# Kernel tuning notes

Hardware: AMD Instinct MI355X
Metric: run time of the kernel (lower is better)

Reference implementation:

```python
import jax, jax.numpy as jnp
import numpy as np

D_MODEL = 1024
NUM_HEADS = 16
DEPTH = D_MODEL // NUM_HEADS
B, S = 4, 1024


def setup_inputs() -> dict:
    key = jax.random.key(0)
    ks = jax.random.split(key, 9)
    scale = 0.02
    return {
        "v": jax.random.normal(ks[0], (B, S, D_MODEL), jnp.float32),
        "k": jax.random.normal(ks[1], (B, S, D_MODEL), jnp.float32),
        "q": jax.random.normal(ks[2], (B, S, D_MODEL), jnp.float32),
        "wq_w": jax.random.normal(ks[3], (D_MODEL, D_MODEL), jnp.float32) * scale,
        "wq_b": jax.random.normal(ks[4], (D_MODEL,), jnp.float32) * scale,
        "wv_w": jax.random.normal(ks[5], (D_MODEL, D_MODEL), jnp.float32) * scale,
        "wv_b": jax.random.normal(ks[6], (D_MODEL,), jnp.float32) * scale,
        "dense_w": jax.random.normal(ks[7], (D_MODEL, D_MODEL), jnp.float32) * scale,
        "dense_b": jax.random.normal(ks[8], (D_MODEL,), jnp.float32) * scale,
    }


def _split_heads(x):
    # [B, S, D] -> [B, H, S, depth]
    b, s, _ = x.shape
    return x.reshape(b, s, NUM_HEADS, DEPTH).transpose(0, 2, 1, 3)


def reference(v, k, q, wq_w, wq_b, wv_w, wv_b, dense_w, dense_b):
    # Faithful to original torch module, including its bugs:
    #   v = wv(v); k = wv(v)  (k input and wk layer unused)
    #   output = logits @ v   (raw logits, NOT softmax weights)
    del k  # unused in original forward (overwritten)
    q_p = q @ wq_w.T + wq_b
    v_p = v @ wv_w.T + wv_b
    k_p = v_p @ wv_w.T + wv_b  # k = self.wv(v) after v already projected

    qh = _split_heads(q_p)  # [B,H,S,dh]
    kh = _split_heads(k_p)
    vh = _split_heads(v_p)

    logits = jnp.einsum("bhsd,bhtd->bhst", qh, kh) / jnp.sqrt(
        jnp.asarray(DEPTH, jnp.float32)
    )  # [B,H,S,S]
    attention_weights = jax.nn.softmax(logits, axis=-1)
    # BUG preserved: uses logits, not attention_weights
    attn_out = jnp.einsum("bhst,bhtd->bhsd", logits, vh)  # [B,H,S,dh]

    concat = attn_out.transpose(0, 2, 1, 3).reshape(B, S, D_MODEL)
    output = concat @ dense_w.T + dense_b
    # dropout is identity in eval mode
    return output, attention_weights
```

## Files before the change

kernel.cpp:

```cpp
#include <hip/hip_runtime.h>
#include <hip/hip_bf16.h>

#define DM 1024
#define BS 4
#define SS 1024
#define NH 16

typedef __attribute__((ext_vector_type(8))) short bf16x8;
typedef __attribute__((ext_vector_type(4))) float f32x4;

__device__ inline unsigned short f2bf(float x) {
    union { float f; unsigned u; } v; v.f = x;
    unsigned r = v.u + 0x7fffu + ((v.u >> 16) & 1u);
    return (unsigned short)(r >> 16);
}
__device__ inline float bf2f(unsigned short u) {
    union { unsigned u; float f; } v; v.u = ((unsigned)u) << 16;
    return v.f;
}

template<typename T> __device__ inline void store1(T* p, float v);
template<> __device__ inline void store1<float>(float* p, float v) { *p = v; }
template<> __device__ inline void store1<unsigned short>(unsigned short* p, float v) { *p = f2bf(v); }

__device__ inline void glds16(const unsigned short* g, unsigned short* l) {
    __builtin_amdgcn_global_load_lds(
        (const __attribute__((address_space(1))) unsigned int*)g,
        (__attribute__((address_space(3))) unsigned int*)l, 16, 0, 0);
}

__global__ __launch_bounds__(256) void cvt_bf16(const float* __restrict__ in,
                                                unsigned short* __restrict__ out, int n4)
{
    int i = blockIdx.x * blockDim.x + threadIdx.x;
    const int stride = gridDim.x * blockDim.x;
    for (; i < n4; i += stride) {
        float4 v = reinterpret_cast<const float4*>(in)[i];
        ushort4 o;
        o.x = f2bf(v.x); o.y = f2bf(v.y); o.z = f2bf(v.z); o.w = f2bf(v.w);
        reinterpret_cast<ushort4*>(out)[i] = o;
    }
}

template<typename TO>
__global__ __launch_bounds__(256) void gemm64_bt(
    const unsigned short* __restrict__ A, int lda,
    const unsigned short* __restrict__ B, int ldb,
    TO* __restrict__ C, int ldc,
    const float* __restrict__ bias, int K, float scale)
{
    __shared__ unsigned short lA[2][64 * 32];
    __shared__ unsigned short lB[2][64 * 32];

    const int tid = threadIdx.x;
    const int wid = tid >> 6, lane = tid & 63;
    const int wr = wid >> 1, wc = wid & 1;
    const int r0 = lane & 15;
    const int kq = (lane >> 4) * 8;
    const int srow = lane >> 2;
    const int scol = (lane & 3) * 8;

    const unsigned short* Ap = A + ((long long)blockIdx.y * 64 + wid * 16 + srow) * lda + scol;
    const unsigned short* Bp = B + ((long long)blockIdx.x * 64 + wid * 16 + srow) * ldb + scol;
    TO* Cp = C + (long long)blockIdx.y * 64 * ldc + blockIdx.x * 64;

    f32x4 acc[2][2];
    #pragma unroll
    for (int m = 0; m < 2; ++m)
        #pragma unroll
        for (int n = 0; n < 2; ++n)
            acc[m][n] = f32x4{0.f, 0.f, 0.f, 0.f};

    glds16(Ap, &lA[0][wid * 512]);
    glds16(Bp, &lB[0][wid * 512]);
    __syncthreads();

    const int NT = K / 32;
    int cur = 0;
    for (int t = 0; t < NT; ++t) {
        if (t + 1 < NT) {
            glds16(Ap + (t + 1) * 32, &lA[cur ^ 1][wid * 512]);
            glds16(Bp + (t + 1) * 32, &lB[cur ^ 1][wid * 512]);
        }
        bf16x8 af[2], bfr[2];
        #pragma unroll
        for (int m = 0; m < 2; ++m)
            af[m] = *reinterpret_cast<const bf16x8*>(&lA[cur][(wr * 32 + m * 16 + r0) * 32 + kq]);
        #pragma unroll
        for (int n = 0; n < 2; ++n)
            bfr[n] = *reinterpret_cast<const bf16x8*>(&lB[cur][(wc * 32 + n * 16 + r0) * 32 + kq]);
        #pragma unroll
        for (int m = 0; m < 2; ++m)
            #pragma unroll
            for (int n = 0; n < 2; ++n)
                acc[m][n] = __builtin_amdgcn_mfma_f32_16x16x32_bf16(af[m], bfr[n], acc[m][n], 0, 0, 0);
        __syncthreads();
        cur ^= 1;
    }

    const int cf = lane & 15, rf = (lane >> 4) * 4;
    #pragma unroll
    for (int m = 0; m < 2; ++m) {
        #pragma unroll
        for (int n = 0; n < 2; ++n) {
            int col = wc * 32 + n * 16 + cf;
            float bv = bias ? bias[blockIdx.x * 64 + col] : 0.0f;
            #pragma unroll
            for (int j = 0; j < 4; ++j) {
                int row = wr * 32 + m * 16 + rf + j;
                store1<TO>(&Cp[(long long)row * ldc + col], acc[m][n][j] * scale + bv);
            }
        }
    }
}

__global__ __launch_bounds__(256) void transpose_vh(const unsigned short* __restrict__ vp,
                                                    unsigned short* __restrict__ vT)
{
    __shared__ unsigned short tile[64][65];
    const int bh = blockIdx.y;
    const int b = bh >> 4, h = bh & 15;
    const long long t0 = (long long)blockIdx.x * 64;
    const int tid = threadIdx.x;
    #pragma unroll
    for (int kk = 0; kk < 4; ++kk) {
        int l = tid + kk * 256;
        int row = l >> 4, c4 = l & 15;
        const unsigned short* src = vp + ((long long)b * SS + t0 + row) * DM + h * 64 + c4 * 4;
        ushort4 val = *reinterpret_cast<const ushort4*>(src);
        tile[row][c4 * 4 + 0] = val.x;
        tile[row][c4 * 4 + 1] = val.y;
        tile[row][c4 * 4 + 2] = val.z;
        tile[row][c4 * 4 + 3] = val.w;
    }
    __syncthreads();
    #pragma unroll
    for (int kk = 0; kk < 4; ++kk) {
        int l = tid + kk * 256;
        int d = l >> 4, i4 = l & 15;
        ushort4 o;
        o.x = tile[i4 * 4 + 0][d];
        o.y = tile[i4 * 4 + 1][d];
        o.z = tile[i4 * 4 + 2][d];
        o.w = tile[i4 * 4 + 3][d];
        *reinterpret_cast<ushort4*>(vT + ((long long)bh * 64 + d) * SS + t0 + i4 * 4) = o;
    }
}

__global__ __launch_bounds__(256, 4) void fused_attn3(
    const unsigned short* __restrict__ qp,
    const unsigned short* __restrict__ kp,
    const unsigned short* __restrict__ vT,
    float* __restrict__ attnw,
    unsigned short* __restrict__ cc)
{
    constexpr int LSTR = 1032;
    __shared__ alignas(16) unsigned short S16[16 * LSTR];
    __shared__ float2 msW[4][16];
    __shared__ float rowM[16];
    __shared__ float rowI[16];

    const int tid = threadIdx.x;
    const int w = tid >> 6;
    const int lane = tid & 63;
    const int lg = lane >> 4;
    const int ln = lane & 15;
    const int z = blockIdx.y, b = z >> 4, h = z & 15;
    const int row0 = blockIdx.x * 16;

    const unsigned short* qbase = qp + ((long long)b * SS + row0) * DM + h * 64;
    const unsigned short* kbase = kp + (long long)b * SS * DM + h * 64;
    const unsigned short* vbase = vT + (long long)z * 64 * SS;

    bf16x8 qf[2];
    #pragma unroll
    for (int ks = 0; ks < 2; ++ks)
        qf[ks] = *reinterpret_cast<const bf16x8*>(qbase + (long long)ln * DM + ks * 32 + lg * 8);

    float m4[4], s4[4];
    #pragma unroll
    for (int j = 0; j < 4; ++j) { m4[j] = -1e30f; s4[j] = 0.f; }

    bf16x8 kf_cur[4];
    #pragma unroll
    for (int i = 0; i < 4; ++i) {
        const int ks = i >> 1, cf2 = i & 1;
        kf_cur[i] = *reinterpret_cast<const bf16x8*>(
            kbase + (long long)(w * 32 + cf2 * 16 + ln) * DM + ks * 32 + lg * 8);
    }
    for (int c = 0; c < 8; ++c) {
        bf16x8 kf_nxt[4];
        if (c < 7) {
            #pragma unroll
            for (int i = 0; i < 4; ++i) {
                const int ks = i >> 1, cf2 = i & 1;
                kf_nxt[i] = *reinterpret_cast<const bf16x8*>(
                    kbase + (long long)((c + 1) * 128 + w * 32 + cf2 * 16 + ln) * DM + ks * 32 + lg * 8);
            }
        }
        f32x4 sac[2];
        sac[0] = f32x4{0.f, 0.f, 0.f, 0.f};
        sac[1] = f32x4{0.f, 0.f, 0.f, 0.f};
        sac[0] = __builtin_amdgcn_mfma_f32_16x16x32_bf16(qf[0], kf_cur[0], sac[0], 0, 0, 0);
        sac[1] = __builtin_amdgcn_mfma_f32_16x16x32_bf16(qf[0], kf_cur[1], sac[1], 0, 0, 0);
        sac[0] = __builtin_amdgcn_mfma_f32_16x16x32_bf16(qf[1], kf_cur[2], sac[0], 0, 0, 0);
        sac[1] = __builtin_amdgcn_mfma_f32_16x16x32_bf16(qf[1], kf_cur[3], sac[1], 0, 0, 0);

        const int colbase = c * 128 + w * 32;
        #pragma unroll
        for (int cf2 = 0; cf2 < 2; ++cf2)
            #pragma unroll
            for (int j = 0; j < 4; ++j) {
                unsigned short ub = f2bf(sac[cf2][j] * 0.125f);
                S16[(lg * 4 + j) * LSTR + colbase + cf2 * 16 + ln] = ub;
                sac[cf2][j] = bf2f(ub);
            }
        #pragma unroll
        for (int j = 0; j < 4; ++j) {
            float v0 = sac[0][j], v1 = sac[1][j];
            float mn = fmaxf(m4[j], fmaxf(v0, v1));
            s4[j] = s4[j] * __expf(m4[j] - mn) + __expf(v0 - mn) + __expf(v1 - mn);
            m4[j] = mn;
        }
        if (c < 7) {
            #pragma unroll
            for (int i = 0; i < 4; ++i) kf_cur[i] = kf_nxt[i];
        }
    }

    #pragma unroll
    for (int j = 0; j < 4; ++j) {
        #pragma unroll
        for (int o = 1; o < 16; o <<= 1) {
            float mo = __shfl_xor(m4[j], o);
            float so = __shfl_xor(s4[j], o);
            float mn = fmaxf(m4[j], mo);
            s4[j] = s4[j] * __expf(m4[j] - mn) + so * __expf(mo - mn);
            m4[j] = mn;
        }
    }
    if (ln == 0) {
        #pragma unroll
        for (int j = 0; j < 4; ++j) msW[w][lg * 4 + j] = make_float2(m4[j], s4[j]);
    }
    __syncthreads();
    if (tid < 16) {
        float mf = -1e30f;
        #pragma unroll
        for (int w2 = 0; w2 < 4; ++w2) mf = fmaxf(mf, msW[w2][tid].x);
        float sf = 0.f;
        #pragma unroll
        for (int w2 = 0; w2 < 4; ++w2) sf += msW[w2][tid].y * __expf(msW[w2][tid].x - mf);
        rowM[tid] = mf;
        rowI[tid] = 1.0f / sf;
    }
    __syncthreads();

    #pragma unroll 4
    for (int it = 0; it < 16; ++it) {
        float mf = rowM[it], inv = rowI[it];
        uint2 sv = *reinterpret_cast<const uint2*>(&S16[it * LSTR + tid * 4]);
        float4 o;
        o.x = __expf(bf2f((unsigned short)(sv.x & 0xffffu)) - mf) * inv;
        o.y = __expf(bf2f((unsigned short)(sv.x >> 16)) - mf) * inv;
        o.z = __expf(bf2f((unsigned short)(sv.y & 0xffffu)) - mf) * inv;
        o.w = __expf(bf2f((unsigned short)(sv.y >> 16)) - mf) * inv;
        *reinterpret_cast<float4*>(attnw + ((long long)z * SS + row0 + it) * SS + tid * 4) = o;
    }

    {
        f32x4 pvn = f32x4{0.f, 0.f, 0.f, 0.f};
        const unsigned short* vrow = vbase + (long long)(w * 16 + ln) * SS;
        for (int kk = 0; kk < 32; ++kk) {
            bf16x8 sa = *reinterpret_cast<const bf16x8*>(&S16[ln * LSTR + kk * 32 + lg * 8]);
            bf16x8 vf = *reinterpret_cast<const bf16x8*>(vrow + kk * 32 + lg * 8);
            pvn = __builtin_amdgcn_mfma_f32_16x16x32_bf16(sa, vf, pvn, 0, 0, 0);
        }
        #pragma unroll
        for (int j = 0; j < 4; ++j)
            cc[((long long)b * SS + row0 + lg * 4 + j) * DM + h * 64 + w * 16 + ln] = f2bf(pvn[j]);
    }
}

extern "C" void kernel_launch(void* const* d_in, const int* in_sizes, int n_in,
                              void* d_out, int out_size, void* d_ws, size_t ws_size,
                              hipStream_t stream) {
    (void)in_sizes; (void)n_in; (void)out_size; (void)ws_size;
    const float* v    = (const float*)d_in[0];
    const float* q    = (const float*)d_in[2];
    const float* wq_w = (const float*)d_in[3];
    const float* wq_b = (const float*)d_in[4];
    const float* wv_w = (const float*)d_in[5];
    const float* wv_b = (const float*)d_in[6];
    const float* dw   = (const float*)d_in[7];
    const float* db   = (const float*)d_in[8];

    unsigned short* q_p = (unsigned short*)d_ws;
    unsigned short* v_p = q_p + (4 << 20);
    unsigned short* k_p = v_p + (4 << 20);
    unsigned short* vT  = k_p + (4 << 20);
    unsigned short* cc  = vT  + (4 << 20);

    float* out0   = (float*)d_out;
    float* attnw  = out0 + (long long)BS * SS * DM;

    unsigned short* qb  = (unsigned short*)attnw;
    unsigned short* vb  = qb  + (4 << 20);
    unsigned short* wqb = vb  + (4 << 20);
    unsigned short* wvb = wqb + (1 << 20);
    unsigned short* dwb = q_p;

    dim3 blk(256);
    dim3 gemmGrid(DM / 64, BS * SS / 64);

    cvt_bf16<<<dim3(1024), blk, 0, stream>>>(q, qb, (BS * SS * DM) / 4);
    cvt_bf16<<<dim3(1024), blk, 0, stream>>>(v, vb, (BS * SS * DM) / 4);
    cvt_bf16<<<dim3(256),  blk, 0, stream>>>(wq_w, wqb, (DM * DM) / 4);
    cvt_bf16<<<dim3(256),  blk, 0, stream>>>(wv_w, wvb, (DM * DM) / 4);

    gemm64_bt<unsigned short><<<gemmGrid, blk, 0, stream>>>(
        qb, DM, wqb, DM, q_p, DM, wq_b, DM, 1.0f);
    gemm64_bt<unsigned short><<<gemmGrid, blk, 0, stream>>>(
        vb, DM, wvb, DM, v_p, DM, wv_b, DM, 1.0f);
    gemm64_bt<unsigned short><<<gemmGrid, blk, 0, stream>>>(
        v_p, DM, wvb, DM, k_p, DM, wv_b, DM, 1.0f);

    transpose_vh<<<dim3(16, 64), blk, 0, stream>>>(v_p, vT);

    fused_attn3<<<dim3(SS / 16, BS * NH), blk, 0, stream>>>(q_p, k_p, vT, attnw, cc);

    cvt_bf16<<<dim3(256), blk, 0, stream>>>(dw, dwb, (DM * DM) / 4);
    gemm64_bt<float><<<gemmGrid, blk, 0, stream>>>(
        cc, DM, dwb, DM, out0, DM, db, DM, 1.0f);
}
```

Measured before the change: 249.3 us.

## Enlarge GEMM M-tile to 128 and attention block to 32 query rows

The GEMM kernel now computes 128x64 output tiles per block, with each wave holding a 64x32 sub-tile, so each loaded B tile is reused across more rows. The fused attention kernel now handles 32 query rows per block with 512 threads, so each K fragment loaded feeds two row-halves of MFMAs and K traffic per query row is halved. The cost is more registers and LDS per block (a 32-row score buffer of about 66KB), fewer blocks in flight, and larger GEMM tiles that halve the grid, which may hurt occupancy.

```diff
diff --git a/kernel.cpp b/kernel.cpp
--- a/kernel.cpp
+++ b/kernel.cpp
@@ -43,13 +43,13 @@
 }
 
 template<typename TO>
-__global__ __launch_bounds__(256) void gemm64_bt(
+__global__ __launch_bounds__(256) void gemm128_bt(
     const unsigned short* __restrict__ A, int lda,
     const unsigned short* __restrict__ B, int ldb,
     TO* __restrict__ C, int ldc,
     const float* __restrict__ bias, int K, float scale)
 {
-    __shared__ unsigned short lA[2][64 * 32];
+    __shared__ unsigned short lA[2][128 * 32];
     __shared__ unsigned short lB[2][64 * 32];
 
     const int tid = threadIdx.x;
@@ -60,37 +60,39 @@
     const int srow = lane >> 2;
     const int scol = (lane & 3) * 8;
 
-    const unsigned short* Ap = A + ((long long)blockIdx.y * 64 + wid * 16 + srow) * lda + scol;
-    const unsigned short* Bp = B + ((long long)blockIdx.x * 64 + wid * 16 + srow) * ldb + scol;
-    TO* Cp = C + (long long)blockIdx.y * 64 * ldc + blockIdx.x * 64;
-
-    f32x4 acc[2][2];
-    #pragma unroll
-    for (int m = 0; m < 2; ++m)
+    const unsigned short* Ap = A + ((long long)blockIdx.y * 128 + srow) * lda + scol;
+    const unsigned short* Bp = B + ((long long)blockIdx.x * 64 + srow) * ldb + scol;
+    TO* Cp = C + (long long)blockIdx.y * 128 * ldc + blockIdx.x * 64;
+
+    f32x4 acc[4][2];
+    #pragma unroll
+    for (int m = 0; m < 4; ++m)
         #pragma unroll
         for (int n = 0; n < 2; ++n)
             acc[m][n] = f32x4{0.f, 0.f, 0.f, 0.f};
 
-    glds16(Ap, &lA[0][wid * 512]);
-    glds16(Bp, &lB[0][wid * 512]);
+    glds16(Ap + (long long)(wid * 32) * lda, &lA[0][wid * 1024]);
+    glds16(Ap + (long long)(wid * 32 + 16) * lda, &lA[0][wid * 1024 + 512]);
+    glds16(Bp + (long long)(wid * 16) * ldb, &lB[0][wid * 512]);
     __syncthreads();
 
     const int NT = K / 32;
     int cur = 0;
     for (int t = 0; t < NT; ++t) {
         if (t + 1 < NT) {
-            glds16(Ap + (t + 1) * 32, &lA[cur ^ 1][wid * 512]);
-            glds16(Bp + (t + 1) * 32, &lB[cur ^ 1][wid * 512]);
-        }
-        bf16x8 af[2], bfr[2];
-        #pragma unroll
-        for (int m = 0; m < 2; ++m)
-            af[m] = *reinterpret_cast<const bf16x8*>(&lA[cur][(wr * 32 + m * 16 + r0) * 32 + kq]);
+            glds16(Ap + (long long)(wid * 32) * lda + (t + 1) * 32, &lA[cur ^ 1][wid * 1024]);
+            glds16(Ap + (long long)(wid * 32 + 16) * lda + (t + 1) * 32, &lA[cur ^ 1][wid * 1024 + 512]);
+            glds16(Bp + (long long)(wid * 16) * ldb + (t + 1) * 32, &lB[cur ^ 1][wid * 512]);
+        }
+        bf16x8 af[4], bfr[2];
+        #pragma unroll
+        for (int m = 0; m < 4; ++m)
+            af[m] = *reinterpret_cast<const bf16x8*>(&lA[cur][(wr * 64 + m * 16 + r0) * 32 + kq]);
         #pragma unroll
         for (int n = 0; n < 2; ++n)
             bfr[n] = *reinterpret_cast<const bf16x8*>(&lB[cur][(wc * 32 + n * 16 + r0) * 32 + kq]);
         #pragma unroll
-        for (int m = 0; m < 2; ++m)
+        for (int m = 0; m < 4; ++m)
             #pragma unroll
             for (int n = 0; n < 2; ++n)
                 acc[m][n] = __builtin_amdgcn_mfma_f32_16x16x32_bf16(af[m], bfr[n], acc[m][n], 0, 0, 0);
@@ -100,14 +102,14 @@
 
     const int cf = lane & 15, rf = (lane >> 4) * 4;
     #pragma unroll
-    for (int m = 0; m < 2; ++m) {
+    for (int m = 0; m < 4; ++m) {
         #pragma unroll
         for (int n = 0; n < 2; ++n) {
             int col = wc * 32 + n * 16 + cf;
             float bv = bias ? bias[blockIdx.x * 64 + col] : 0.0f;
             #pragma unroll
             for (int j = 0; j < 4; ++j) {
-                int row = wr * 32 + m * 16 + rf + j;
+                int row = wr * 64 + m * 16 + rf + j;
                 store1<TO>(&Cp[(long long)row * ldc + col], acc[m][n][j] * scale + bv);
             }
         }
@@ -147,7 +149,7 @@
     }
 }
 
-__global__ __launch_bounds__(256, 4) void fused_attn3(
+__global__ __launch_bounds__(512, 4) void fused_attn4(
     const unsigned short* __restrict__ qp,
     const unsigned short* __restrict__ kp,
     const unsigned short* __restrict__ vT,
@@ -155,10 +157,10 @@
     unsigned short* __restrict__ cc)
 {
     constexpr int LSTR = 1032;
-    __shared__ alignas(16) unsigned short S16[16 * LSTR];
-    __shared__ float2 msW[4][16];
-    __shared__ float rowM[16];
-    __shared__ float rowI[16];
+    __shared__ alignas(16) unsigned short S16[32 * LSTR];
+    __shared__ float2 msW[8][32];
+    __shared__ float rowM[32];
+    __shared__ float rowI[32];
 
     const int tid = threadIdx.x;
     const int w = tid >> 6;
@@ -166,20 +168,25 @@
     const int lg = lane >> 4;
     const int ln = lane & 15;
     const int z = blockIdx.y, b = z >> 4, h = z & 15;
-    const int row0 = blockIdx.x * 16;
+    const int row0 = blockIdx.x * 32;
 
     const unsigned short* qbase = qp + ((long long)b * SS + row0) * DM + h * 64;
     const unsigned short* kbase = kp + (long long)b * SS * DM + h * 64;
     const unsigned short* vbase = vT + (long long)z * 64 * SS;
 
-    bf16x8 qf[2];
-    #pragma unroll
-    for (int ks = 0; ks < 2; ++ks)
-        qf[ks] = *reinterpret_cast<const bf16x8*>(qbase + (long long)ln * DM + ks * 32 + lg * 8);
-
-    float m4[4], s4[4];
-    #pragma unroll
-    for (int j = 0; j < 4; ++j) { m4[j] = -1e30f; s4[j] = 0.f; }
+    bf16x8 qf[2][2];
+    #pragma unroll
+    for (int rh = 0; rh < 2; ++rh)
+        #pragma unroll
+        for (int ks = 0; ks < 2; ++ks)
+            qf[rh][ks] = *reinterpret_cast<const bf16x8*>(
+                qbase + (long long)(rh * 16 + ln) * DM + ks * 32 + lg * 8);
+
+    float m4[2][4], s4[2][4];
+    #pragma unroll
+    for (int rh = 0; rh < 2; ++rh)
+        #pragma unroll
+        for (int j = 0; j < 4; ++j) { m4[rh][j] = -1e30f; s4[rh][j] = 0.f; }
 
     bf16x8 kf_cur[4];
     #pragma unroll
@@ -188,97 +195,118 @@
         kf_cur[i] = *reinterpret_cast<const bf16x8*>(
             kbase + (long long)(w * 32 + cf2 * 16 + ln) * DM + ks * 32 + lg * 8);
     }
-    for (int c = 0; c < 8; ++c) {
+    for (int c = 0; c < 4; ++c) {
         bf16x8 kf_nxt[4];
-        if (c < 7) {
+        if (c < 3) {
             #pragma unroll
             for (int i = 0; i < 4; ++i) {
                 const int ks = i >> 1, cf2 = i & 1;
                 kf_nxt[i] = *reinterpret_cast<const bf16x8*>(
-                    kbase + (long long)((c + 1) * 128 + w * 32 + cf2 * 16 + ln) * DM + ks * 32 + lg * 8);
+                    kbase + (long long)((c + 1) * 256 + w * 32 + cf2 * 16 + ln) * DM + ks * 32 + lg * 8);
             }
         }
-        f32x4 sac[2];
-        sac[0] = f32x4{0.f, 0.f, 0.f, 0.f};
-        sac[1] = f32x4{0.f, 0.f, 0.f, 0.f};
-        sac[0] = __builtin_amdgcn_mfma_f32_16x16x32_bf16(qf[0], kf_cur[0], sac[0], 0, 0, 0);
-        sac[1] = __builtin_amdgcn_mfma_f32_16x16x32_bf16(qf[0], kf_cur[1], sac[1], 0, 0, 0);
-        sac[0] = __builtin_amdgcn_mfma_f32_16x16x32_bf16(qf[1], kf_cur[2], sac[0], 0, 0, 0);
-        sac[1] = __builtin_amdgcn_mfma_f32_16x16x32_bf16(qf[1], kf_cur[3], sac[1], 0, 0, 0);
-
-        const int colbase = c * 128 + w * 32;
-        #pragma unroll
-        for (int cf2 = 0; cf2 < 2; ++cf2)
+        f32x4 sac[2][2];
+        #pragma unroll
+        for (int rh = 0; rh < 2; ++rh) {
+            sac[rh][0] = f32x4{0.f, 0.f, 0.f, 0.f};
+            sac[rh][1] = f32x4{0.f, 0.f, 0.f, 0.f};
+        }
+        #pragma unroll
+        for (int ks = 0; ks < 2; ++ks)
+            #pragma unroll
+            for (int cf2 = 0; cf2 < 2; ++cf2)
+                #pragma unroll
+                for (int rh = 0; rh < 2; ++rh)
+                    sac[rh][cf2] = __builtin_amdgcn_mfma_f32_16x16x32_bf16(
+                        qf[rh][ks], kf_cur[ks * 2 + cf2], sac[rh][cf2], 0, 0, 0);
+
+        const int colbase = c * 256 + w * 32;
+        #pragma unroll
+        for (int rh = 0; rh < 2; ++rh) {
+            #pragma unroll
+            for (int cf2 = 0; cf2 < 2; ++cf2)
+                #pragma unroll
+                for (int j = 0; j < 4; ++j) {
+                    unsigned short ub = f2bf(sac[rh][cf2][j] * 0.125f);
+                    S16[(rh * 16 + lg * 4 + j) * LSTR + colbase + cf2 * 16 + ln] = ub;
+                    sac[rh][cf2][j] = bf2f(ub);
+                }
             #pragma unroll
             for (int j = 0; j < 4; ++j) {
-                unsigned short ub = f2bf(sac[cf2][j] * 0.125f);
-                S16[(lg * 4 + j) * LSTR + colbase + cf2 * 16 + ln] = ub;
-                sac[cf2][j] = bf2f(ub);
+                float v0 = sac[rh][0][j], v1 = sac[rh][1][j];
+                float mn = fmaxf(m4[rh][j], fmaxf(v0, v1));
+                s4[rh][j] = s4[rh][j] * __expf(m4[rh][j] - mn) + __expf(v0 - mn) + __expf(v1 - mn);
+                m4[rh][j] = mn;
             }
+        }
+        if (c < 3) {
+            #pragma unroll
+            for (int i = 0; i < 4; ++i) kf_cur[i] = kf_nxt[i];
+        }
+    }
+
+    #pragma unroll
+    for (int rh = 0; rh < 2; ++rh)
         #pragma unroll
         for (int j = 0; j < 4; ++j) {
-            float v0 = sac[0][j], v1 = sac[1][j];
-            float mn = fmaxf(m4[j], fmaxf(v0, v1));
-            s4[j] = s4[j] * __expf(m4[j] - mn) + __expf(v0 - mn) + __expf(v1 - mn);
-            m4[j] = mn;
-        }
-        if (c < 7) {
-            #pragma unroll
-            for (int i = 0; i < 4; ++i) kf_cur[i] = kf_nxt[i];
-        }
-    }
-
-    #pragma unroll
-    for (int j = 0; j < 4; ++j) {
-        #pragma unroll
-        for (int o = 1; o < 16; o <<= 1) {
-            float mo = __shfl_xor(m4[j], o);
-            float so = __shfl_xor(s4[j], o);
-            float mn = fmaxf(m4[j], mo);
-            s4[j] = s4[j] * __expf(m4[j] - mn) + so * __expf(mo - mn);
-            m4[j] = mn;
-        }
-    }
+            #pragma unroll
+            for (int o = 1; o < 16; o <<= 1) {
+                float mo = __shfl_xor(m4[rh][j], o);
+                float so = __shfl_xor(s4[rh][j], o);
+                float mn = fmaxf(m4[rh][j], mo);
+                s4[rh][j] = s4[rh][j] * __expf(m4[rh][j] - mn) + so * __expf(mo - mn);
+                m4[rh][j] = mn;
+            }
+        }
     if (ln == 0) {
         #pragma unroll
-        for (int j = 0; j < 4; ++j) msW[w][lg * 4 + j] = make_float2(m4[j], s4[j]);
+        for (int rh = 0; rh < 2; ++rh)
+            #pragma unroll
+            for (int j = 0; j < 4; ++j)
+                msW[w][rh * 16 + lg * 4 + j] = make_float2(m4[rh][j], s4[rh][j]);
     }
     __syncthreads();
-    if (tid < 16) {
+    if (tid < 32) {
         float mf = -1e30f;
         #pragma unroll
-        for (int w2 = 0; w2 < 4; ++w2) mf = fmaxf(mf, msW[w2][tid].x);
+        for (int w2 = 0; w2 < 8; ++w2) mf = fmaxf(mf, msW[w2][tid].x);
         float sf = 0.f;
         #pragma unroll
-        for (int w2 = 0; w2 < 4; ++w2) sf += msW[w2][tid].y * __expf(msW[w2][tid].x - mf);
+        for (int w2 = 0; w2 < 8; ++w2) sf += msW[w2][tid].y * __expf(msW[w2][tid].x - mf);
         rowM[tid] = mf;
         rowI[tid] = 1.0f / sf;
     }
     __syncthreads();
 
-    #pragma unroll 4
-    for (int it = 0; it < 16; ++it) {
-        float mf = rowM[it], inv = rowI[it];
-        uint2 sv = *reinterpret_cast<const uint2*>(&S16[it * LSTR + tid * 4]);
-        float4 o;
-        o.x = __expf(bf2f((unsigned short)(sv.x & 0xffffu)) - mf) * inv;
-        o.y = __expf(bf2f((unsigned short)(sv.x >> 16)) - mf) * inv;
-        o.z = __expf(bf2f((unsigned short)(sv.y & 0xffffu)) - mf) * inv;
-        o.w = __expf(bf2f((unsigned short)(sv.y >> 16)) - mf) * inv;
-        *reinterpret_cast<float4*>(attnw + ((long long)z * SS + row0 + it) * SS + tid * 4) = o;
-    }
-
     {
+        const int rr = tid >> 8;
+        const int tcol = tid & 255;
+        #pragma unroll 4
+        for (int it = 0; it < 16; ++it) {
+            const int row = it * 2 + rr;
+            float mf = rowM[row], inv = rowI[row];
+            uint2 sv = *reinterpret_cast<const uint2*>(&S16[row * LSTR + tcol * 4]);
+            float4 o;
+            o.x = __expf(bf2f((unsigned short)(sv.x & 0xffffu)) - mf) * inv;
+            o.y = __expf(bf2f((unsigned short)(sv.x >> 16)) - mf) * inv;
+            o.z = __expf(bf2f((unsigned short)(sv.y & 0xffffu)) - mf) * inv;
+            o.w = __expf(bf2f((unsigned short)(sv.y >> 16)) - mf) * inv;
+            *reinterpret_cast<float4*>(attnw + ((long long)z * SS + row0 + row) * SS + tcol * 4) = o;
+        }
+    }
+
+    {
+        const int rh = w >> 2, ds = w & 3;
         f32x4 pvn = f32x4{0.f, 0.f, 0.f, 0.f};
-        const unsigned short* vrow = vbase + (long long)(w * 16 + ln) * SS;
+        const unsigned short* vrow = vbase + (long long)(ds * 16 + ln) * SS;
         for (int kk = 0; kk < 32; ++kk) {
-            bf16x8 sa = *reinterpret_cast<const bf16x8*>(&S16[ln * LSTR + kk * 32 + lg * 8]);
+            bf16x8 sa = *reinterpret_cast<const bf16x8*>(&S16[(rh * 16 + ln) * LSTR + kk * 32 + lg * 8]);
             bf16x8 vf = *reinterpret_cast<const bf16x8*>(vrow + kk * 32 + lg * 8);
             pvn = __builtin_amdgcn_mfma_f32_16x16x32_bf16(sa, vf, pvn, 0, 0, 0);
         }
         #pragma unroll
         for (int j = 0; j < 4; ++j)
-            cc[((long long)b * SS + row0 + lg * 4 + j) * DM + h * 64 + w * 16 + ln] = f2bf(pvn[j]);
+            cc[((long long)b * SS + row0 + rh * 16 + lg * 4 + j) * DM + h * 64 + ds * 16 + ln] = f2bf(pvn[j]);
     }
 }
 
@@ -311,25 +339,25 @@
     unsigned short* dwb = q_p;
 
     dim3 blk(256);
-    dim3 gemmGrid(DM / 64, BS * SS / 64);
+    dim3 gemmGrid(DM / 64, BS * SS / 128);
 
     cvt_bf16<<<dim3(1024), blk, 0, stream>>>(q, qb, (BS * SS * DM) / 4);
     cvt_bf16<<<dim3(1024), blk, 0, stream>>>(v, vb, (BS * SS * DM) / 4);
     cvt_bf16<<<dim3(256),  blk, 0, stream>>>(wq_w, wqb, (DM * DM) / 4);
     cvt_bf16<<<dim3(256),  blk, 0, stream>>>(wv_w, wvb, (DM * DM) / 4);
 
-    gemm64_bt<unsigned short><<<gemmGrid, blk, 0, stream>>>(
+    gemm128_bt<unsigned short><<<gemmGrid, blk, 0, stream>>>(
         qb, DM, wqb, DM, q_p, DM, wq_b, DM, 1.0f);
-    gemm64_bt<unsigned short><<<gemmGrid, blk, 0, stream>>>(
+    gemm128_bt<unsigned short><<<gemmGrid, blk, 0, stream>>>(
         vb, DM, wvb, DM, v_p, DM, wv_b, DM, 1.0f);
-    gemm64_bt<unsigned short><<<gemmGrid, blk, 0, stream>>>(
+    gemm128_bt<unsigned short><<<gemmGrid, blk, 0, stream>>>(
         v_p, DM, wvb, DM, k_p, DM, wv_b, DM, 1.0f);
 
     transpose_vh<<<dim3(16, 64), blk, 0, stream>>>(v_p, vT);
 
-    fused_attn3<<<dim3(SS / 16, BS * NH), blk, 0, stream>>>(q_p, k_p, vT, attnw, cc);
+    fused_attn4<<<dim3(SS / 32, BS * NH), dim3(512), 0, stream>>>(q_p, k_p, vT, attnw, cc);
 
     cvt_bf16<<<dim3(256), blk, 0, stream>>>(dw, dwb, (DM * DM) / 4);
-    gemm64_bt<float><<<gemmGrid, blk, 0, stream>>>(
+    gemm128_bt<float><<<gemmGrid, blk, 0, stream>>>(
         cc, DM, dwb, DM, out0, DM, db, DM, 1.0f);
 }
```

After: 246.0 us. No clear change (-1.3%).
